# Kernel optimization log

Measured on AMD Instinct MI355X. Metric: run time of the kernel, lower is better.

Reference implementation:

```python
import math
import jax, jax.numpy as jnp
import numpy as np

BS, Q_LEN, DIM = 8, 16, 4096
MAX_SEQ = 4096
N_Q_HEADS, N_KV_HEADS, HEAD_DIM = 32, 8, 128
REP = N_Q_HEADS // N_KV_HEADS


def setup_inputs() -> dict:
    key = jax.random.key(0)
    ks = jax.random.split(key, 12)
    w = 0.02
    return {
        "x": jax.random.normal(ks[0], (BS, Q_LEN, DIM), jnp.float32),
        "k_cache": jax.random.normal(ks[1], (BS, MAX_SEQ, N_KV_HEADS, HEAD_DIM), jnp.float32),
        "v_cache": jax.random.normal(ks[2], (BS, MAX_SEQ, N_KV_HEADS, HEAD_DIM), jnp.float32),
        "Wq": jax.random.normal(ks[3], (DIM, N_Q_HEADS * HEAD_DIM), jnp.float32) * w,
        "bq": jax.random.normal(ks[4], (N_Q_HEADS * HEAD_DIM,), jnp.float32) * w,
        "Wk": jax.random.normal(ks[5], (DIM, N_KV_HEADS * HEAD_DIM), jnp.float32) * w,
        "bk": jax.random.normal(ks[6], (N_KV_HEADS * HEAD_DIM,), jnp.float32) * w,
        "Wv": jax.random.normal(ks[7], (DIM, N_KV_HEADS * HEAD_DIM), jnp.float32) * w,
        "bv": jax.random.normal(ks[8], (N_KV_HEADS * HEAD_DIM,), jnp.float32) * w,
        "Wo": jax.random.normal(ks[9], (N_Q_HEADS * HEAD_DIM, DIM), jnp.float32) * w,
        "bo": jax.random.normal(ks[10], (DIM,), jnp.float32) * w,
        "start_pos": MAX_SEQ - Q_LEN,
        "seq_len_for_kv": Q_LEN,
    }


def reference(x, k_cache, v_cache, Wq, bq, Wk, bk, Wv, bv, Wo, bo, start_pos, seq_len_for_kv):
    bs, sl, dim = x.shape
    # Projections (torch Linear: x @ W^T + b; here W stored as [in, out])
    q = (x @ Wq + bq).reshape(bs, sl, N_KV_HEADS, REP, HEAD_DIM)  # [b, q, g, r, d]
    k = (x @ Wk + bk).reshape(bs, sl, N_KV_HEADS, HEAD_DIM)
    v = (x @ Wv + bv).reshape(bs, sl, N_KV_HEADS, HEAD_DIM)
    # KV-cache append (start_pos / seq_len_for_kv are static Python ints)
    k_cache = k_cache.at[:, start_pos:start_pos + seq_len_for_kv].set(k)
    v_cache = v_cache.at[:, start_pos:start_pos + seq_len_for_kv].set(v)
    kv_len = start_pos + seq_len_for_kv
    keys = k_cache[:, :kv_len]    # [b, L, g, d]
    vals = v_cache[:, :kv_len]    # [b, L, g, d]
    # GQA: each kv head g serves REP query heads r (broadcast instead of repeat_kv)
    scale = 1.0 / math.sqrt(HEAD_DIM)
    scores = jnp.einsum('bqgrd,blgd->bgrql', q, keys) * scale  # [b, g, r, q, L]
    att = jax.nn.softmax(scores, axis=-1)
    out = jnp.einsum('bgrql,blgd->bqgrd', att, vals)           # [b, q, g, r, d]
    out = out.reshape(bs, sl, N_Q_HEADS * HEAD_DIM)
    return out @ Wo + bo
```

## Files before the change

kernel.cpp:

```cpp
#include <hip/hip_runtime.h>
#include <math.h>

#define DIM       4096
#define NKVH      8
#define HD        128
#define MAX_SEQ   4096
#define START_POS 4080
#define NQKV      6144
#define NCHUNK    8
#define CHUNK     512
#define KS        8
#define ATT_SCALE 0.08838834764831845f

#define WS_PART   0
#define WS_QH     6291456
#define WS_QL     6553600
#define WS_KNEW   6815744
#define WS_VNEW   6946816
#define WS_PM     7077888
#define WS_PL     7110656
#define WS_ATH    7143424
#define WS_ATL    7405568
#define WS_XH     7667712
#define WS_XL     7929856
#define WS_PARTO  WS_PART

typedef __bf16 bf16x8 __attribute__((ext_vector_type(8)));
typedef float  f32x4  __attribute__((ext_vector_type(4)));
typedef unsigned int uintx4 __attribute__((ext_vector_type(4)));

__device__ __forceinline__ unsigned short f2bf(float f) {
    return __builtin_bit_cast(unsigned short, (__bf16)f);
}
__device__ __forceinline__ float bf2f(unsigned short h) {
    union { unsigned int u; float f; } v; v.u = ((unsigned int)h) << 16;
    return v.f;
}
__device__ __forceinline__ void splitbf(float f, unsigned short &h, unsigned short &l) {
    h = f2bf(f);
    l = f2bf(f - bf2f(h));
}
__device__ __forceinline__ bf16x8 ldsfrag(const unsigned short* p) {
    uintx4 u = *(const uintx4*)p;
    return __builtin_bit_cast(bf16x8, u);
}
__device__ __forceinline__ bf16x8 ldsfrag2(const unsigned short* p) {
    union { uint2 u2[2]; bf16x8 v; } u;
    u.u2[0] = *(const uint2*)p;
    u.u2[1] = *(const uint2*)(p + 4);
    return u.v;
}
#define MFMA16(a,b,c) __builtin_amdgcn_mfma_f32_16x16x32_bf16(a, b, c, 0, 0, 0)
#define VCOMP(v,j) ((j)==0?(v).x:((j)==1?(v).y:((j)==2?(v).z:(v).w)))

__global__ __launch_bounds__(256) void split_x_kernel(
    const float* __restrict__ x, unsigned short* __restrict__ xh,
    unsigned short* __restrict__ xl, int n)
{
    int i = blockIdx.x * 256 + threadIdx.x;
    if (i < n) { unsigned short h, l; splitbf(x[i], h, l); xh[i] = h; xl[i] = l; }
}

__device__ __forceinline__ void gemm_body(
    const unsigned short* __restrict__ Ah, const unsigned short* __restrict__ Al,
    const float* __restrict__ W, int ldW, int noff,
    float* __restrict__ part, int partStride, int ncol0, int ks,
    unsigned short* Ahs, unsigned short* Als, unsigned short* Bs)
{
    const int t = threadIdx.x;
    const int w = t >> 6, lane = t & 63, l15 = lane & 15, quad = lane >> 4;
    f32x4 acc[2][4];
    #pragma unroll
    for (int i = 0; i < 2; ++i)
        #pragma unroll
        for (int nt = 0; nt < 4; ++nt) acc[i][nt] = (f32x4){0.f, 0.f, 0.f, 0.f};

    const int k0base = ks * 512;
    uintx4 areg_h[4], areg_l[4];
    float4 wreg[4];

    auto LOAD = [&](int it) {
        int k0 = k0base + it * 64;
        #pragma unroll
        for (int i = 0; i < 4; ++i) {
            int f = t + i * 256;
            int row = f >> 3, c0 = (f & 7) << 3;
            size_t off = (size_t)row * DIM + k0 + c0;
            areg_h[i] = *(const uintx4*)(Ah + off);
            areg_l[i] = *(const uintx4*)(Al + off);
        }
        #pragma unroll
        for (int i = 0; i < 4; ++i) {
            int kk = (t >> 4) + 16 * i;
            int n0 = (t & 15) << 2;
            wreg[i] = *(const float4*)(W + (size_t)(k0 + kk) * ldW + noff + n0);
        }
    };

    LOAD(0);
    for (int it = 0; it < 8; ++it) {
        __syncthreads();
        #pragma unroll
        for (int i = 0; i < 4; ++i) {
            int f = t + i * 256;
            int row = f >> 3, c0 = (f & 7) << 3;
            *(uintx4*)(Ahs + row * 72 + c0) = areg_h[i];
            *(uintx4*)(Als + row * 72 + c0) = areg_l[i];
        }
        {
            int n0 = (t & 15) << 2;
            #pragma unroll
            for (int i = 0; i < 4; ++i) {
                int kk = (t >> 4) + 16 * i;
                #pragma unroll
                for (int j = 0; j < 4; ++j)
                    Bs[(n0 + j) * 68 + kk] = f2bf(VCOMP(wreg[i], j));
            }
        }
        __syncthreads();
        if (it < 7) LOAD(it + 1);
        #pragma unroll
        for (int kt = 0; kt < 2; ++kt) {
            int ko = kt * 32 + quad * 8;
            bf16x8 ah0 = ldsfrag(Ahs + ((2*w+0)*16 + l15) * 72 + ko);
            bf16x8 ah1 = ldsfrag(Ahs + ((2*w+1)*16 + l15) * 72 + ko);
            bf16x8 al0 = ldsfrag(Als + ((2*w+0)*16 + l15) * 72 + ko);
            bf16x8 al1 = ldsfrag(Als + ((2*w+1)*16 + l15) * 72 + ko);
            #pragma unroll
            for (int nt = 0; nt < 4; ++nt) {
                bf16x8 b = ldsfrag2(Bs + (nt*16 + l15) * 68 + ko);
                acc[0][nt] = MFMA16(ah0, b, acc[0][nt]);
                acc[0][nt] = MFMA16(al0, b, acc[0][nt]);
                acc[1][nt] = MFMA16(ah1, b, acc[1][nt]);
                acc[1][nt] = MFMA16(al1, b, acc[1][nt]);
            }
        }
    }
    #pragma unroll
    for (int i = 0; i < 2; ++i)
        #pragma unroll
        for (int nt = 0; nt < 4; ++nt)
            #pragma unroll
            for (int r = 0; r < 4; ++r) {
                int row = (2*w + i) * 16 + quad * 4 + r;
                int col = ncol0 + nt * 16 + l15;
                part[(size_t)(ks * 128 + row) * partStride + col] = acc[i][nt][r];
            }
}

__global__ __launch_bounds__(256) void qkv_gemm_kernel(
    const unsigned short* __restrict__ xh, const unsigned short* __restrict__ xl,
    const float* __restrict__ Wq, const float* __restrict__ Wk,
    const float* __restrict__ Wv, float* __restrict__ part)
{
    __shared__ unsigned short Ahs[128 * 72], Als[128 * 72];
    __shared__ unsigned short Bs[64 * 68];
    int ncol0 = blockIdx.x * 64;
    int ks = blockIdx.y;
    const float* W; int ldW, noff;
    if (ncol0 < 4096)      { W = Wq; ldW = 4096; noff = ncol0; }
    else if (ncol0 < 5120) { W = Wk; ldW = 1024; noff = ncol0 - 4096; }
    else                   { W = Wv; ldW = 1024; noff = ncol0 - 5120; }
    gemm_body(xh, xl, W, ldW, noff, part, NQKV, ncol0, ks, Ahs, Als, Bs);
}

__global__ __launch_bounds__(256) void oproj_gemm_kernel(
    const unsigned short* __restrict__ ah, const unsigned short* __restrict__ al,
    const float* __restrict__ Wo, float* __restrict__ part)
{
    __shared__ unsigned short Ahs[128 * 72], Als[128 * 72];
    __shared__ unsigned short Bs[64 * 68];
    int ncol0 = blockIdx.x * 64;
    int ks = blockIdx.y;
    gemm_body(ah, al, Wo, 4096, ncol0, part, 4096, ncol0, ks, Ahs, Als, Bs);
}

__global__ __launch_bounds__(256) void qkv_reduce_kernel(
    const float* __restrict__ part, const float* __restrict__ bq,
    const float* __restrict__ bk, const float* __restrict__ bv,
    unsigned short* __restrict__ qh, unsigned short* __restrict__ ql,
    float* __restrict__ k_new, float* __restrict__ v_new)
{
    int gid = blockIdx.x * 256 + threadIdx.x;
    int row = gid / NQKV;
    int n   = gid - row * NQKV;
    float s = 0.f;
    #pragma unroll
    for (int j = 0; j < KS; ++j)
        s += part[(size_t)(j * 128 + row) * NQKV + n];
    if (n < 4096) {
        float v = s + bq[n];
        unsigned short h, l; splitbf(v, h, l);
        qh[row * 4096 + n] = h; ql[row * 4096 + n] = l;
    } else if (n < 5120) k_new[row * 1024 + (n - 4096)] = s + bk[n - 4096];
    else                 v_new[row * 1024 + (n - 5120)] = s + bv[n - 5120];
}

__global__ __launch_bounds__(512, 2) void attn_partial5_kernel(
    const unsigned short* __restrict__ qhp, const unsigned short* __restrict__ qlp,
    const float* __restrict__ kc, const float* __restrict__ vc,
    const float* __restrict__ knew, const float* __restrict__ vnew,
    float* __restrict__ part_O, float* __restrict__ part_m, float* __restrict__ part_l)
{
    __shared__ unsigned short Kb[2][32][136];
    __shared__ unsigned short Vt[2][128][44];
    __shared__ unsigned short Pw[8][16 * 36];

    const int t = threadIdx.x;
    const int w = t >> 6, lane = t & 63, l15 = lane & 15, quad = lane >> 4;
    const int gsel = w >> 2;
    const int rep  = w & 3;
    const int blk = blockIdx.x;
    const int b = blk >> 5, gg = (blk >> 3) & 3, c = blk & 7;
    const int g = gg * 2 + gsel;

    const int p0 = t >> 6;
    const int q4 = t & 63;
    const int gl = q4 >> 5;
    const int d0 = (q4 & 31) << 2;

    bf16x8 qhf[4], qlf[4];
    {
        size_t base = (size_t)(b * 16 + l15) * DIM + (g * 4 + rep) * HD + quad * 8;
        #pragma unroll
        for (int kt = 0; kt < 4; ++kt) {
            qhf[kt] = ldsfrag(qhp + base + kt * 32);
            qlf[kt] = ldsfrag(qlp + base + kt * 32);
        }
    }

    float m_run[4], l_run[4];
    f32x4 oacc[8];
    #pragma unroll
    for (int r = 0; r < 4; ++r) { m_run[r] = -INFINITY; l_run[r] = 0.f; }
    #pragma unroll
    for (int d = 0; d < 8; ++d) oacc[d] = (f32x4){0.f, 0.f, 0.f, 0.f};

    float4 kreg[4], vreg[4];
    auto LOADKV = [&](int it) {
        #pragma unroll
        for (int i = 0; i < 4; ++i) {
            int pos = p0 + i * 8;
            int pg = c * CHUNK + it * 32 + pos;
            const float *ksrc, *vsrc;
            if (pg >= START_POS) {
                size_t off = (size_t)(b * 16 + pg - START_POS) * (NKVH * HD) + gg * 256 + q4 * 4;
                ksrc = knew + off; vsrc = vnew + off;
            } else {
                size_t off = ((size_t)(b * MAX_SEQ + pg) * NKVH) * HD + gg * 256 + q4 * 4;
                ksrc = kc + off; vsrc = vc + off;
            }
            kreg[i] = *(const float4*)ksrc;
            vreg[i] = *(const float4*)vsrc;
        }
    };

    unsigned short* phw = Pw[w];

    LOADKV(0);
    for (int it = 0; it < 16; ++it) {
        __syncthreads();
        #pragma unroll
        for (int i = 0; i < 4; ++i) {
            int pos = p0 + i * 8;
            ushort4 k4 = make_ushort4(f2bf(kreg[i].x), f2bf(kreg[i].y),
                                      f2bf(kreg[i].z), f2bf(kreg[i].w));
            *(ushort4*)&Kb[gl][pos][d0] = k4;
        }
        #pragma unroll
        for (int j = 0; j < 4; ++j) {
            ushort4 v4 = make_ushort4(f2bf(VCOMP(vreg[0], j)), f2bf(VCOMP(vreg[1], j)),
                                      f2bf(VCOMP(vreg[2], j)), f2bf(VCOMP(vreg[3], j)));
            *(ushort4*)&Vt[gl][d0 + j][p0 * 4] = v4;
        }
        __syncthreads();
        if (it + 1 < 16) LOADKV(it + 1);

        f32x4 sacc[2];
        sacc[0] = (f32x4){0.f,0.f,0.f,0.f};
        sacc[1] = (f32x4){0.f,0.f,0.f,0.f};
        #pragma unroll
        for (int nt = 0; nt < 2; ++nt)
            #pragma unroll
            for (int kt = 0; kt < 4; ++kt) {
                bf16x8 bh = ldsfrag(&Kb[gsel][nt*16 + l15][kt*32 + quad*8]);
                sacc[nt] = MFMA16(qhf[kt], bh, sacc[nt]);
                sacc[nt] = MFMA16(qlf[kt], bh, sacc[nt]);
            }

        float e0[4], e1[4], alpha[4];
        #pragma unroll
        for (int r = 0; r < 4; ++r) {
            float s0 = sacc[0][r] * ATT_SCALE;
            float s1 = sacc[1][r] * ATT_SCALE;
            float mx = fmaxf(s0, s1);
            mx = fmaxf(mx, __shfl_xor(mx, 1));
            mx = fmaxf(mx, __shfl_xor(mx, 2));
            mx = fmaxf(mx, __shfl_xor(mx, 4));
            mx = fmaxf(mx, __shfl_xor(mx, 8));
            float mnew = fmaxf(m_run[r], mx);
            alpha[r] = __expf(m_run[r] - mnew);
            e0[r] = __expf(s0 - mnew);
            e1[r] = __expf(s1 - mnew);
            float sum = e0[r] + e1[r];
            sum += __shfl_xor(sum, 1);
            sum += __shfl_xor(sum, 2);
            sum += __shfl_xor(sum, 4);
            sum += __shfl_xor(sum, 8);
            l_run[r] = l_run[r] * alpha[r] + sum;
            m_run[r] = mnew;
        }
        #pragma unroll
        for (int d = 0; d < 8; ++d)
            #pragma unroll
            for (int r = 0; r < 4; ++r) oacc[d][r] *= alpha[r];

        {
            int slot0 = 4 * (l15 & 7) + (l15 >> 3);
            #pragma unroll
            for (int r = 0; r < 4; ++r) {
                phw[(quad*4 + r) * 36 + slot0]     = f2bf(e0[r]);
                phw[(quad*4 + r) * 36 + slot0 + 2] = f2bf(e1[r]);
            }
        }
        bf16x8 pa = ldsfrag(phw + l15 * 36 + quad * 8);

        #pragma unroll
        for (int dt = 0; dt < 8; ++dt) {
            bf16x8 vb = ldsfrag(&Vt[gsel][dt*16 + l15][quad * 8]);
            oacc[dt] = MFMA16(pa, vb, oacc[dt]);
        }
    }

    const size_t obase = (size_t)((b * 8 + g) * 8 + c) * 64 + rep * 16 + quad * 4;
    #pragma unroll
    for (int dt = 0; dt < 8; ++dt)
        #pragma unroll
        for (int r = 0; r < 4; ++r)
            part_O[(obase + r) * HD + dt * 16 + l15] = oacc[dt][r];
    if (l15 == 0) {
        #pragma unroll
        for (int r = 0; r < 4; ++r) {
            part_m[obase + r] = m_run[r];
            part_l[obase + r] = l_run[r];
        }
    }
}

__global__ __launch_bounds__(128) void attn_combine_kernel(
    const float* __restrict__ part_O, const float* __restrict__ part_m,
    const float* __restrict__ part_l, unsigned short* __restrict__ ah,
    unsigned short* __restrict__ al)
{
    int bid = blockIdx.x;
    int d = threadIdx.x;
    int bg = bid >> 6;
    int row = bid & 63;
    float mc[NCHUNK], lc[NCHUNK];
    float M = -INFINITY;
    #pragma unroll
    for (int cc = 0; cc < NCHUNK; ++cc) {
        mc[cc] = part_m[(bg * NCHUNK + cc) * 64 + row];
        lc[cc] = part_l[(bg * NCHUNK + cc) * 64 + row];
        M = fmaxf(M, mc[cc]);
    }
    float L = 0.f, acc = 0.f;
    #pragma unroll
    for (int cc = 0; cc < NCHUNK; ++cc) {
        float wgt = __expf(mc[cc] - M);
        L += lc[cc] * wgt;
        acc += part_O[((size_t)(bg * NCHUNK + cc) * 64 + row) * HD + d] * wgt;
    }
    int b = bg >> 3, g = bg & 7;
    int r = row >> 4, qp = row & 15;
    float v = acc / L;
    unsigned short h, l; splitbf(v, h, l);
    size_t idx = (size_t)(b * 16 + qp) * DIM + (g * 4 + r) * HD + d;
    ah[idx] = h; al[idx] = l;
}

__global__ __launch_bounds__(256) void oproj_reduce_kernel(
    const float* __restrict__ part, const float* __restrict__ bo,
    float* __restrict__ out)
{
    int gid = blockIdx.x * 256 + threadIdx.x;
    int n = gid & 4095;
    float s = 0.f;
    #pragma unroll
    for (int j = 0; j < KS; ++j) s += part[(size_t)j * 524288 + gid];
    out[gid] = s + bo[n];
}

extern "C" void kernel_launch(void* const* d_in, const int* in_sizes, int n_in,
                              void* d_out, int out_size, void* d_ws, size_t ws_size,
                              hipStream_t stream)
{
    const float* x  = (const float*)d_in[0];
    const float* kc = (const float*)d_in[1];
    const float* vc = (const float*)d_in[2];
    const float* Wq = (const float*)d_in[3];
    const float* bq = (const float*)d_in[4];
    const float* Wk = (const float*)d_in[5];
    const float* bk = (const float*)d_in[6];
    const float* Wv = (const float*)d_in[7];
    const float* bv = (const float*)d_in[8];
    const float* Wo = (const float*)d_in[9];
    const float* bo = (const float*)d_in[10];
    float* out = (float*)d_out;
    float* ws  = (float*)d_ws;

    unsigned short* xh = (unsigned short*)(ws + WS_XH);
    unsigned short* xl = (unsigned short*)(ws + WS_XL);
    unsigned short* qh = (unsigned short*)(ws + WS_QH);
    unsigned short* ql = (unsigned short*)(ws + WS_QL);
    unsigned short* ath = (unsigned short*)(ws + WS_ATH);
    unsigned short* atl = (unsigned short*)(ws + WS_ATL);

    split_x_kernel<<<2048, 256, 0, stream>>>(x, xh, xl, 524288);
    qkv_gemm_kernel<<<dim3(96, KS), 256, 0, stream>>>(xh, xl, Wq, Wk, Wv, ws + WS_PART);
    qkv_reduce_kernel<<<3072, 256, 0, stream>>>(ws + WS_PART, bq, bk, bv,
                                                qh, ql, ws + WS_KNEW, ws + WS_VNEW);
    attn_partial5_kernel<<<256, 512, 0, stream>>>(qh, ql, kc, vc,
                                                  ws + WS_KNEW, ws + WS_VNEW,
                                                  ws + WS_PARTO, ws + WS_PM, ws + WS_PL);
    attn_combine_kernel<<<4096, 128, 0, stream>>>(ws + WS_PARTO, ws + WS_PM,
                                                  ws + WS_PL, ath, atl);
    oproj_gemm_kernel<<<dim3(64, KS), 256, 0, stream>>>(ath, atl, Wo, ws + WS_PART);
    oproj_reduce_kernel<<<2048, 256, 0, stream>>>(ws + WS_PART, bo, out);
}
```

Before: 438.9 us.

## Widen GEMM column tiles, vectorize elementwise kernels, double-buffer attention KV loads

The GEMM body is templated on the number of column tiles, so QKV uses 256-wide and O-proj 128-wide blocks. Each block now reuses its staged A (x hi/lo) tile across more columns, which cuts redundant A reads, but the launches drop to far fewer blocks (24x8 and 32x8). The split, QKV-reduce and O-reduce kernels now work on float4/ushort4 per thread. The attention kernel keeps two KV register sets so the next chunk's global loads overlap compute. The tradeoffs are more register and LDS use, and much lower block-level parallelism on a GPU with many CUs.

```diff
diff --git a/kernel.cpp b/kernel.cpp
--- a/kernel.cpp
+++ b/kernel.cpp
@@ -55,70 +55,78 @@
 
 __global__ __launch_bounds__(256) void split_x_kernel(
     const float* __restrict__ x, unsigned short* __restrict__ xh,
-    unsigned short* __restrict__ xl, int n)
+    unsigned short* __restrict__ xl, int n4)
 {
     int i = blockIdx.x * 256 + threadIdx.x;
-    if (i < n) { unsigned short h, l; splitbf(x[i], h, l); xh[i] = h; xl[i] = l; }
-}
-
+    if (i < n4) {
+        float4 v = *(const float4*)(x + (size_t)i * 4);
+        ushort4 h, l;
+        splitbf(v.x, h.x, l.x);
+        splitbf(v.y, h.y, l.y);
+        splitbf(v.z, h.z, l.z);
+        splitbf(v.w, h.w, l.w);
+        *(ushort4*)(xh + (size_t)i * 4) = h;
+        *(ushort4*)(xl + (size_t)i * 4) = l;
+    }
+}
+
+template<int NT>
 __device__ __forceinline__ void gemm_body(
     const unsigned short* __restrict__ Ah, const unsigned short* __restrict__ Al,
     const float* __restrict__ W, int ldW, int noff,
     float* __restrict__ part, int partStride, int ncol0, int ks,
     unsigned short* Ahs, unsigned short* Als, unsigned short* Bs)
 {
+    constexpr int NC4   = NT * 4;
+    constexpr int RSTEP = 256 / NC4;
     const int t = threadIdx.x;
     const int w = t >> 6, lane = t & 63, l15 = lane & 15, quad = lane >> 4;
-    f32x4 acc[2][4];
+    const int n4 = t & (NC4 - 1);
+    const int kk = t / NC4;
+
+    f32x4 acc[2][NT];
     #pragma unroll
     for (int i = 0; i < 2; ++i)
         #pragma unroll
-        for (int nt = 0; nt < 4; ++nt) acc[i][nt] = (f32x4){0.f, 0.f, 0.f, 0.f};
+        for (int nt = 0; nt < NT; ++nt) acc[i][nt] = (f32x4){0.f, 0.f, 0.f, 0.f};
 
     const int k0base = ks * 512;
-    uintx4 areg_h[4], areg_l[4];
-    float4 wreg[4];
-
-    auto LOAD = [&](int it) {
+    float4 wreg[NT];
+
+    auto LOADW = [&](int it) {
         int k0 = k0base + it * 64;
+        #pragma unroll
+        for (int i = 0; i < NT; ++i)
+            wreg[i] = *(const float4*)(W + (size_t)(k0 + kk + RSTEP * i) * ldW + noff + n4 * 4);
+    };
+
+    LOADW(0);
+    for (int it = 0; it < 8; ++it) {
+        int k0 = k0base + it * 64;
+        __syncthreads();
+        uintx4 ah4[4], al4[4];
         #pragma unroll
         for (int i = 0; i < 4; ++i) {
             int f = t + i * 256;
             int row = f >> 3, c0 = (f & 7) << 3;
             size_t off = (size_t)row * DIM + k0 + c0;
-            areg_h[i] = *(const uintx4*)(Ah + off);
-            areg_l[i] = *(const uintx4*)(Al + off);
-        }
-        #pragma unroll
-        for (int i = 0; i < 4; ++i) {
-            int kk = (t >> 4) + 16 * i;
-            int n0 = (t & 15) << 2;
-            wreg[i] = *(const float4*)(W + (size_t)(k0 + kk) * ldW + noff + n0);
-        }
-    };
-
-    LOAD(0);
-    for (int it = 0; it < 8; ++it) {
-        __syncthreads();
+            ah4[i] = *(const uintx4*)(Ah + off);
+            al4[i] = *(const uintx4*)(Al + off);
+        }
+        #pragma unroll
+        for (int i = 0; i < NT; ++i)
+            #pragma unroll
+            for (int j = 0; j < 4; ++j)
+                Bs[(n4 * 4 + j) * 68 + kk + RSTEP * i] = f2bf(VCOMP(wreg[i], j));
         #pragma unroll
         for (int i = 0; i < 4; ++i) {
             int f = t + i * 256;
             int row = f >> 3, c0 = (f & 7) << 3;
-            *(uintx4*)(Ahs + row * 72 + c0) = areg_h[i];
-            *(uintx4*)(Als + row * 72 + c0) = areg_l[i];
-        }
-        {
-            int n0 = (t & 15) << 2;
-            #pragma unroll
-            for (int i = 0; i < 4; ++i) {
-                int kk = (t >> 4) + 16 * i;
-                #pragma unroll
-                for (int j = 0; j < 4; ++j)
-                    Bs[(n0 + j) * 68 + kk] = f2bf(VCOMP(wreg[i], j));
-            }
-        }
-        __syncthreads();
-        if (it < 7) LOAD(it + 1);
+            *(uintx4*)(Ahs + row * 72 + c0) = ah4[i];
+            *(uintx4*)(Als + row * 72 + c0) = al4[i];
+        }
+        __syncthreads();
+        if (it < 7) LOADW(it + 1);
         #pragma unroll
         for (int kt = 0; kt < 2; ++kt) {
             int ko = kt * 32 + quad * 8;
@@ -127,7 +135,7 @@
             bf16x8 al0 = ldsfrag(Als + ((2*w+0)*16 + l15) * 72 + ko);
             bf16x8 al1 = ldsfrag(Als + ((2*w+1)*16 + l15) * 72 + ko);
             #pragma unroll
-            for (int nt = 0; nt < 4; ++nt) {
+            for (int nt = 0; nt < NT; ++nt) {
                 bf16x8 b = ldsfrag2(Bs + (nt*16 + l15) * 68 + ko);
                 acc[0][nt] = MFMA16(ah0, b, acc[0][nt]);
                 acc[0][nt] = MFMA16(al0, b, acc[0][nt]);
@@ -139,7 +147,7 @@
     #pragma unroll
     for (int i = 0; i < 2; ++i)
         #pragma unroll
-        for (int nt = 0; nt < 4; ++nt)
+        for (int nt = 0; nt < NT; ++nt)
             #pragma unroll
             for (int r = 0; r < 4; ++r) {
                 int row = (2*w + i) * 16 + quad * 4 + r;
@@ -148,31 +156,31 @@
             }
 }
 
-__global__ __launch_bounds__(256) void qkv_gemm_kernel(
+__global__ __launch_bounds__(256, 2) void qkv_gemm_kernel(
     const unsigned short* __restrict__ xh, const unsigned short* __restrict__ xl,
     const float* __restrict__ Wq, const float* __restrict__ Wk,
     const float* __restrict__ Wv, float* __restrict__ part)
 {
     __shared__ unsigned short Ahs[128 * 72], Als[128 * 72];
-    __shared__ unsigned short Bs[64 * 68];
-    int ncol0 = blockIdx.x * 64;
+    __shared__ unsigned short Bs[256 * 68];
+    int ncol0 = blockIdx.x * 256;
     int ks = blockIdx.y;
     const float* W; int ldW, noff;
     if (ncol0 < 4096)      { W = Wq; ldW = 4096; noff = ncol0; }
     else if (ncol0 < 5120) { W = Wk; ldW = 1024; noff = ncol0 - 4096; }
     else                   { W = Wv; ldW = 1024; noff = ncol0 - 5120; }
-    gemm_body(xh, xl, W, ldW, noff, part, NQKV, ncol0, ks, Ahs, Als, Bs);
-}
-
-__global__ __launch_bounds__(256) void oproj_gemm_kernel(
+    gemm_body<16>(xh, xl, W, ldW, noff, part, NQKV, ncol0, ks, Ahs, Als, Bs);
+}
+
+__global__ __launch_bounds__(256, 2) void oproj_gemm_kernel(
     const unsigned short* __restrict__ ah, const unsigned short* __restrict__ al,
     const float* __restrict__ Wo, float* __restrict__ part)
 {
     __shared__ unsigned short Ahs[128 * 72], Als[128 * 72];
-    __shared__ unsigned short Bs[64 * 68];
-    int ncol0 = blockIdx.x * 64;
+    __shared__ unsigned short Bs[128 * 68];
+    int ncol0 = blockIdx.x * 128;
     int ks = blockIdx.y;
-    gemm_body(ah, al, Wo, 4096, ncol0, part, 4096, ncol0, ks, Ahs, Als, Bs);
+    gemm_body<8>(ah, al, Wo, 4096, ncol0, part, 4096, ncol0, ks, Ahs, Als, Bs);
 }
 
 __global__ __launch_bounds__(256) void qkv_reduce_kernel(
@@ -182,21 +190,36 @@
     float* __restrict__ k_new, float* __restrict__ v_new)
 {
     int gid = blockIdx.x * 256 + threadIdx.x;
-    int row = gid / NQKV;
-    int n   = gid - row * NQKV;
-    float s = 0.f;
-    #pragma unroll
-    for (int j = 0; j < KS; ++j)
-        s += part[(size_t)(j * 128 + row) * NQKV + n];
+    int row = gid / 1536;
+    int c4  = gid - row * 1536;
+    int n = c4 * 4;
+    float4 s = make_float4(0.f, 0.f, 0.f, 0.f);
+    #pragma unroll
+    for (int j = 0; j < KS; ++j) {
+        float4 p = *(const float4*)&part[(size_t)(j * 128 + row) * NQKV + n];
+        s.x += p.x; s.y += p.y; s.z += p.z; s.w += p.w;
+    }
     if (n < 4096) {
-        float v = s + bq[n];
-        unsigned short h, l; splitbf(v, h, l);
-        qh[row * 4096 + n] = h; ql[row * 4096 + n] = l;
-    } else if (n < 5120) k_new[row * 1024 + (n - 4096)] = s + bk[n - 4096];
-    else                 v_new[row * 1024 + (n - 5120)] = s + bv[n - 5120];
-}
-
-__global__ __launch_bounds__(512, 2) void attn_partial5_kernel(
+        float4 b4 = *(const float4*)&bq[n];
+        ushort4 h, l;
+        splitbf(s.x + b4.x, h.x, l.x);
+        splitbf(s.y + b4.y, h.y, l.y);
+        splitbf(s.z + b4.z, h.z, l.z);
+        splitbf(s.w + b4.w, h.w, l.w);
+        *(ushort4*)&qh[row * 4096 + n] = h;
+        *(ushort4*)&ql[row * 4096 + n] = l;
+    } else if (n < 5120) {
+        float4 b4 = *(const float4*)&bk[n - 4096];
+        float4 o = make_float4(s.x + b4.x, s.y + b4.y, s.z + b4.z, s.w + b4.w);
+        *(float4*)&k_new[row * 1024 + (n - 4096)] = o;
+    } else {
+        float4 b4 = *(const float4*)&bv[n - 5120];
+        float4 o = make_float4(s.x + b4.x, s.y + b4.y, s.z + b4.z, s.w + b4.w);
+        *(float4*)&v_new[row * 1024 + (n - 5120)] = o;
+    }
+}
+
+__global__ __launch_bounds__(512, 2) void attn_partial6_kernel(
     const unsigned short* __restrict__ qhp, const unsigned short* __restrict__ qlp,
     const float* __restrict__ kc, const float* __restrict__ vc,
     const float* __restrict__ knew, const float* __restrict__ vnew,
@@ -236,8 +259,9 @@
     #pragma unroll
     for (int d = 0; d < 8; ++d) oacc[d] = (f32x4){0.f, 0.f, 0.f, 0.f};
 
-    float4 kreg[4], vreg[4];
-    auto LOADKV = [&](int it) {
+    float4 kA[4], vA[4], kB[4], vB[4];
+
+    auto LOADKV = [&](float4 (&kr)[4], float4 (&vr)[4], int it) {
         #pragma unroll
         for (int i = 0; i < 4; ++i) {
             int pos = p0 + i * 8;
@@ -250,32 +274,30 @@
                 size_t off = ((size_t)(b * MAX_SEQ + pg) * NKVH) * HD + gg * 256 + q4 * 4;
                 ksrc = kc + off; vsrc = vc + off;
             }
-            kreg[i] = *(const float4*)ksrc;
-            vreg[i] = *(const float4*)vsrc;
+            kr[i] = *(const float4*)ksrc;
+            vr[i] = *(const float4*)vsrc;
         }
     };
 
-    unsigned short* phw = Pw[w];
-
-    LOADKV(0);
-    for (int it = 0; it < 16; ++it) {
-        __syncthreads();
+    auto STAGE = [&](const float4 (&kr)[4], const float4 (&vr)[4]) {
         #pragma unroll
         for (int i = 0; i < 4; ++i) {
             int pos = p0 + i * 8;
-            ushort4 k4 = make_ushort4(f2bf(kreg[i].x), f2bf(kreg[i].y),
-                                      f2bf(kreg[i].z), f2bf(kreg[i].w));
+            ushort4 k4 = make_ushort4(f2bf(kr[i].x), f2bf(kr[i].y),
+                                      f2bf(kr[i].z), f2bf(kr[i].w));
             *(ushort4*)&Kb[gl][pos][d0] = k4;
         }
         #pragma unroll
         for (int j = 0; j < 4; ++j) {
-            ushort4 v4 = make_ushort4(f2bf(VCOMP(vreg[0], j)), f2bf(VCOMP(vreg[1], j)),
-                                      f2bf(VCOMP(vreg[2], j)), f2bf(VCOMP(vreg[3], j)));
+            ushort4 v4 = make_ushort4(f2bf(VCOMP(vr[0], j)), f2bf(VCOMP(vr[1], j)),
+                                      f2bf(VCOMP(vr[2], j)), f2bf(VCOMP(vr[3], j)));
             *(ushort4*)&Vt[gl][d0 + j][p0 * 4] = v4;
         }
-        __syncthreads();
-        if (it + 1 < 16) LOADKV(it + 1);
-
+    };
+
+    unsigned short* phw = Pw[w];
+
+    auto COMPUTE = [&]() {
         f32x4 sacc[2];
         sacc[0] = (f32x4){0.f,0.f,0.f,0.f};
         sacc[1] = (f32x4){0.f,0.f,0.f,0.f};
@@ -330,6 +352,21 @@
             bf16x8 vb = ldsfrag(&Vt[gsel][dt*16 + l15][quad * 8]);
             oacc[dt] = MFMA16(pa, vb, oacc[dt]);
         }
+    };
+
+    LOADKV(kA, vA, 0);
+    LOADKV(kB, vB, 1);
+    for (int ii = 0; ii < 8; ++ii) {
+        __syncthreads();
+        STAGE(kA, vA);
+        __syncthreads();
+        if (ii < 7) LOADKV(kA, vA, 2*ii + 2);
+        COMPUTE();
+        __syncthreads();
+        STAGE(kB, vB);
+        __syncthreads();
+        if (ii < 7) LOADKV(kB, vB, 2*ii + 3);
+        COMPUTE();
     }
 
     const size_t obase = (size_t)((b * 8 + g) * 8 + c) * 64 + rep * 16 + quad * 4;
@@ -383,12 +420,17 @@
     const float* __restrict__ part, const float* __restrict__ bo,
     float* __restrict__ out)
 {
-    int gid = blockIdx.x * 256 + threadIdx.x;
-    int n = gid & 4095;
-    float s = 0.f;
-    #pragma unroll
-    for (int j = 0; j < KS; ++j) s += part[(size_t)j * 524288 + gid];
-    out[gid] = s + bo[n];
+    int gid4 = blockIdx.x * 256 + threadIdx.x;
+    int n = (gid4 & 1023) * 4;
+    float4 s = make_float4(0.f, 0.f, 0.f, 0.f);
+    #pragma unroll
+    for (int j = 0; j < KS; ++j) {
+        float4 p = *(const float4*)&part[(size_t)j * 524288 + (size_t)gid4 * 4];
+        s.x += p.x; s.y += p.y; s.z += p.z; s.w += p.w;
+    }
+    float4 b4 = *(const float4*)&bo[n];
+    float4 o = make_float4(s.x + b4.x, s.y + b4.y, s.z + b4.z, s.w + b4.w);
+    *(float4*)&out[(size_t)gid4 * 4] = o;
 }
 
 extern "C" void kernel_launch(void* const* d_in, const int* in_sizes, int n_in,
@@ -416,15 +458,15 @@
     unsigned short* ath = (unsigned short*)(ws + WS_ATH);
     unsigned short* atl = (unsigned short*)(ws + WS_ATL);
 
-    split_x_kernel<<<2048, 256, 0, stream>>>(x, xh, xl, 524288);
-    qkv_gemm_kernel<<<dim3(96, KS), 256, 0, stream>>>(xh, xl, Wq, Wk, Wv, ws + WS_PART);
-    qkv_reduce_kernel<<<3072, 256, 0, stream>>>(ws + WS_PART, bq, bk, bv,
-                                                qh, ql, ws + WS_KNEW, ws + WS_VNEW);
-    attn_partial5_kernel<<<256, 512, 0, stream>>>(qh, ql, kc, vc,
+    split_x_kernel<<<512, 256, 0, stream>>>(x, xh, xl, 131072);
+    qkv_gemm_kernel<<<dim3(24, KS), 256, 0, stream>>>(xh, xl, Wq, Wk, Wv, ws + WS_PART);
+    qkv_reduce_kernel<<<768, 256, 0, stream>>>(ws + WS_PART, bq, bk, bv,
+                                               qh, ql, ws + WS_KNEW, ws + WS_VNEW);
+    attn_partial6_kernel<<<256, 512, 0, stream>>>(qh, ql, kc, vc,
                                                   ws + WS_KNEW, ws + WS_VNEW,
                                                   ws + WS_PARTO, ws + WS_PM, ws + WS_PL);
     attn_combine_kernel<<<4096, 128, 0, stream>>>(ws + WS_PARTO, ws + WS_PM,
                                                   ws + WS_PL, ath, atl);
-    oproj_gemm_kernel<<<dim3(64, KS), 256, 0, stream>>>(ath, atl, Wo, ws + WS_PART);
-    oproj_reduce_kernel<<<2048, 256, 0, stream>>>(ws + WS_PART, bo, out);
-}
+    oproj_gemm_kernel<<<dim3(32, KS), 256, 0, stream>>>(ath, atl, Wo, ws + WS_PART);
+    oproj_reduce_kernel<<<512, 256, 0, stream>>>(ws + WS_PART, bo, out);
+}
```

Result: slower. 457.8 us (+4.3%).
